# Performance work log

Measured on AMD Instinct MI355X. Metric: run time of the kernel, lower is better.

The kernel has to match this reference:

```python
import jax, jax.numpy as jnp
from jax import lax
import numpy as np

T, N, H, E, R, L, VOCAB = 512, 200, 64, 16, 10, 2, 200


def setup_inputs() -> dict:
    key = jax.random.key(0)
    ks = jax.random.split(key, 20)
    s = 0.1
    return {
        "inputs": jax.random.normal(ks[0], (T, N), jnp.float32),
        "indices": jnp.arange(N, dtype=jnp.int64) % VOCAB,
        "embed_W": jax.random.normal(ks[1], (VOCAB, E), jnp.float32),
        "Wih0": jax.random.normal(ks[2], (4 * H, 1), jnp.float32) * s,
        "Whh0": jax.random.normal(ks[3], (4 * H, H), jnp.float32) * s,
        "bih0": jax.random.normal(ks[4], (4 * H,), jnp.float32) * s,
        "bhh0": jax.random.normal(ks[5], (4 * H,), jnp.float32) * s,
        "Wih1": jax.random.normal(ks[6], (4 * H, H), jnp.float32) * s,
        "Whh1": jax.random.normal(ks[7], (4 * H, H), jnp.float32) * s,
        "bih1": jax.random.normal(ks[8], (4 * H,), jnp.float32) * s,
        "bhh1": jax.random.normal(ks[9], (4 * H,), jnp.float32) * s,
        "Wm": jax.random.normal(ks[10], (H + E, 1), jnp.float32) * s,
        "bm": jnp.zeros((1,), jnp.float32),
        "Wv": jax.random.normal(ks[11], (H + E, R), jnp.float32) * s,
        "bv": jnp.zeros((R,), jnp.float32),
        "Wd": jax.random.normal(ks[12], (H + E, 1), jnp.float32) * s,
        "bd": jnp.zeros((1,), jnp.float32),
    }


def _cell(x, h, c, Wih, Whh, bih, bhh):
    # PyTorch LSTM cell, gate order i, f, g, o
    g = x @ Wih.T + bih + h @ Whh.T + bhh
    i, f, gg, o = jnp.split(g, 4, axis=-1)
    c_new = jax.nn.sigmoid(f) * c + jax.nn.sigmoid(i) * jnp.tanh(gg)
    h_new = jax.nn.sigmoid(o) * jnp.tanh(c_new)
    return h_new, c_new


def reference(inputs, indices, embed_W, Wih0, Whh0, bih0, bhh0,
              Wih1, Whh1, bih1, bhh1, Wm, bm, Wv, bv, Wd, bd):
    Tn, Nn = inputs.shape
    Hh = Whh0.shape[1]
    layers = [(Wih0, Whh0, bih0, bhh0), (Wih1, Whh1, bih1, bhh1)]
    h0 = jnp.zeros((len(layers), Nn, Hh), inputs.dtype)
    c0 = jnp.zeros_like(h0)

    def step(carry, x_t):
        h, c = carry              # [L, N, H]
        x = x_t[:, None]          # [N, 1] -- assets batched along batch dim
        hs, cs = [], []
        for l, (Wih, Whh, bih, bhh) in enumerate(layers):
            hn, cn = _cell(x, h[l], c[l], Wih, Whh, bih, bhh)
            hs.append(hn)
            cs.append(cn)
            x = hn
        return (jnp.stack(hs), jnp.stack(cs)), x

    _, out = lax.scan(step, (h0, c0), inputs)          # [T, N, H]
    emb = embed_W[indices]                              # [N, E]
    y = jnp.concatenate(
        [out, jnp.broadcast_to(emb[None], (Tn,) + emb.shape)], axis=-1
    )                                                   # [T, N, H+E]
    mu_t = y @ Wm + bm                                  # [T, N, 1]
    d_t = jax.nn.softplus(y @ Wd + bd)[..., 0]          # [T, N]
    v_t = y @ Wv + bv                                   # [T, N, R]
    eye = jnp.eye(Nn, dtype=inputs.dtype)
    cov_t = jnp.einsum('tnr,tmr->tnm', v_t, v_t) + d_t[:, :, None] * eye
    return mu_t, cov_t
```

## Files before the change

### kernel.cpp

```cpp
#include <hip/hip_runtime.h>
#include <hip/hip_bf16.h>
#include <math.h>

#define TT 512
#define NN 200
#define HH 64
#define EE 16
#define RR 10
#define MU_OFF 0
#define COV_OFF (TT*NN)
#define HBLK (NN*NN)
#define HPAD 68

__device__ __forceinline__ float sigmoidf_(float x) {
    return 1.0f / (1.0f + __expf(-x));
}
__device__ __forceinline__ float tanhf_(float x) {
    x = fminf(15.0f, fmaxf(-15.0f, x));
    float e = __expf(2.0f * x);
    return (e - 1.0f) / (e + 1.0f);
}
__device__ __forceinline__ float act_(float g, bool is_tanh) {
    float xx = is_tanh ? 2.0f * g : g;
    float e = __expf(-xx);
    float v = 1.0f / (1.0f + e);
    return is_tanh ? fmaf(2.0f, v, -1.0f) : v;
}

__device__ __forceinline__ float dppxor1(float v) {
    return __int_as_float(__builtin_amdgcn_mov_dpp(__float_as_int(v), 0xB1, 0xf, 0xf, true));
}
__device__ __forceinline__ float dppxor2(float v) {
    return __int_as_float(__builtin_amdgcn_mov_dpp(__float_as_int(v), 0x4E, 0xf, 0xf, true));
}

#define BAR() do { asm volatile("s_waitcnt lgkmcnt(0)" ::: "memory"); \
                   __builtin_amdgcn_s_barrier();                      \
                   asm volatile("" ::: "memory"); } while (0)

#define PIN4(v) asm volatile("" : "+v"(v.x), "+v"(v.y), "+v"(v.z), "+v"(v.w))
#define RM4(M) M(0) M(1) M(2) M(3)

__global__
__attribute__((amdgpu_flat_work_group_size(512, 512), amdgpu_waves_per_eu(2, 2)))
void lstm_kernel(
    const float* __restrict__ inputs,
    const float* __restrict__ Wih0, const float* __restrict__ Whh0,
    const float* __restrict__ bih0, const float* __restrict__ bhh0,
    const float* __restrict__ Wih1, const float* __restrict__ Whh1,
    const float* __restrict__ bih1, const float* __restrict__ bhh1,
    float* __restrict__ out)
{
    const int n = blockIdx.x;
    const int tid = threadIdx.x;

    __shared__ float xs[TT];
    __shared__ float h0s[HH];
    __shared__ float h1s[HH];
    __shared__ float ga0[256];
    __shared__ float ga1[256];
    __shared__ float hist[64][HPAD];

    xs[tid] = inputs[tid * NN + n];
    if (tid < HH) { h0s[tid] = 0.0f; h1s[tid] = 0.0f; }

    float* covbase = out + COV_OFF + n * HH;

    if (tid < 256) {
        const int b4 = tid & ~3;
        const int qr = tid & 3;
#define DECLA(m) \
        float4 wA##m##_0, wA##m##_1, wA##m##_2, wA##m##_3; \
        { const float4* p = (const float4*)(Whh0 + (b4 + m) * HH + qr * 16); \
          wA##m##_0 = p[0]; wA##m##_1 = p[1]; wA##m##_2 = p[2]; wA##m##_3 = p[3]; \
          PIN4(wA##m##_0); PIN4(wA##m##_1); PIN4(wA##m##_2); PIN4(wA##m##_3); }
        RM4(DECLA)
#define DECLAB(m) const float wx##m = Wih0[b4 + m]; \
                  const float bb##m = bih0[b4 + m] + bhh0[b4 + m];
        RM4(DECLAB)
        const bool is_t = ((tid >> 6) == 2);
        const bool upd = (tid < HH);
        float c0 = 0.0f;

        BAR();

        for (int t = 0; t <= TT; ++t) {
            if (t < TT) {
                const float x = xs[t];
                const float4* hq = (const float4*)(h0s + qr * 16);
                float4 hc0 = hq[0], hc1 = hq[1], hc2 = hq[2], hc3 = hq[3];
                float acc0, acc1, acc2, acc3;
#define MVA(m) { \
                float a = (qr == 0) ? fmaf(wx##m, x, bb##m) : 0.0f; \
                a = fmaf(wA##m##_0.x, hc0.x, a); \
                a = fmaf(wA##m##_0.y, hc0.y, a); \
                a = fmaf(wA##m##_0.z, hc0.z, a); \
                a = fmaf(wA##m##_0.w, hc0.w, a); \
                a = fmaf(wA##m##_1.x, hc1.x, a); \
                a = fmaf(wA##m##_1.y, hc1.y, a); \
                a = fmaf(wA##m##_1.z, hc1.z, a); \
                a = fmaf(wA##m##_1.w, hc1.w, a); \
                a = fmaf(wA##m##_2.x, hc2.x, a); \
                a = fmaf(wA##m##_2.y, hc2.y, a); \
                a = fmaf(wA##m##_2.z, hc2.z, a); \
                a = fmaf(wA##m##_2.w, hc2.w, a); \
                a = fmaf(wA##m##_3.x, hc3.x, a); \
                a = fmaf(wA##m##_3.y, hc3.y, a); \
                a = fmaf(wA##m##_3.z, hc3.z, a); \
                a = fmaf(wA##m##_3.w, hc3.w, a); \
                acc##m = a; }
                RM4(MVA)
                acc0 += dppxor1(acc0); acc0 += dppxor2(acc0);
                acc1 += dppxor1(acc1); acc1 += dppxor2(acc1);
                acc2 += dppxor1(acc2); acc2 += dppxor2(acc2);
                acc3 += dppxor1(acc3); acc3 += dppxor2(acc3);
                float g = (qr == 0) ? acc0 : (qr == 1) ? acc1 : (qr == 2) ? acc2 : acc3;
                ga0[tid] = act_(g, is_t);
            }
            BAR();
            if (t < TT && upd) {
                float ia = ga0[tid], fa = ga0[tid + 64];
                float gg = ga0[tid + 128], oa = ga0[tid + 192];
                c0 = fmaf(fa, c0, ia * gg);
                h0s[tid] = oa * tanhf_(c0);
            }
            BAR();
            if ((t & 63) == 0 && t > 0) {
                const int s = tid >> 3;
                const int c = (tid & 7) * 8;
                float4 v0 = *(const float4*)&hist[s][c];
                float4 v1 = *(const float4*)&hist[s][c + 4];
                float* dst = covbase + (size_t)(t - 64 + s) * HBLK + c;
                ((float4*)dst)[0] = v0;
                ((float4*)dst)[1] = v1;
            }
        }
    } else {
        const int r = tid - 256;
        const int b4 = r & ~3;
        const int qr = r & 3;
#define DECLB(m) \
        float4 wI##m##_0, wI##m##_1, wI##m##_2, wI##m##_3; \
        float4 wH##m##_0, wH##m##_1, wH##m##_2, wH##m##_3; \
        { const float4* p = (const float4*)(Wih1 + (b4 + m) * HH + qr * 16); \
          wI##m##_0 = p[0]; wI##m##_1 = p[1]; wI##m##_2 = p[2]; wI##m##_3 = p[3]; \
          PIN4(wI##m##_0); PIN4(wI##m##_1); PIN4(wI##m##_2); PIN4(wI##m##_3); \
          const float4* q2 = (const float4*)(Whh1 + (b4 + m) * HH + qr * 16); \
          wH##m##_0 = q2[0]; wH##m##_1 = q2[1]; wH##m##_2 = q2[2]; wH##m##_3 = q2[3]; \
          PIN4(wH##m##_0); PIN4(wH##m##_1); PIN4(wH##m##_2); PIN4(wH##m##_3); }
        RM4(DECLB)
#define DECLBB(m) const float bB##m = bih1[b4 + m] + bhh1[b4 + m];
        RM4(DECLBB)
        const bool is_t = ((r >> 6) == 2);
        const bool upd = (r < HH);
        float c1 = 0.0f;

        BAR();

        for (int t = 0; t <= TT; ++t) {
            if (t >= 1) {
                const float4* hq = (const float4*)(h0s + qr * 16);
                const float4* gq = (const float4*)(h1s + qr * 16);
                float4 xc0 = hq[0], xc1 = hq[1], xc2 = hq[2], xc3 = hq[3];
                float4 yc0 = gq[0], yc1 = gq[1], yc2 = gq[2], yc3 = gq[3];
                float acc0, acc1, acc2, acc3;
#define MVB(m) { \
                float a = (qr == 0) ? bB##m : 0.0f; \
                float s2 = 0.0f; \
                a  = fmaf(wI##m##_0.x, xc0.x, a); \
                a  = fmaf(wI##m##_0.y, xc0.y, a); \
                a  = fmaf(wI##m##_0.z, xc0.z, a); \
                a  = fmaf(wI##m##_0.w, xc0.w, a); \
                a  = fmaf(wI##m##_1.x, xc1.x, a); \
                a  = fmaf(wI##m##_1.y, xc1.y, a); \
                a  = fmaf(wI##m##_1.z, xc1.z, a); \
                a  = fmaf(wI##m##_1.w, xc1.w, a); \
                a  = fmaf(wI##m##_2.x, xc2.x, a); \
                a  = fmaf(wI##m##_2.y, xc2.y, a); \
                a  = fmaf(wI##m##_2.z, xc2.z, a); \
                a  = fmaf(wI##m##_2.w, xc2.w, a); \
                a  = fmaf(wI##m##_3.x, xc3.x, a); \
                a  = fmaf(wI##m##_3.y, xc3.y, a); \
                a  = fmaf(wI##m##_3.z, xc3.z, a); \
                a  = fmaf(wI##m##_3.w, xc3.w, a); \
                s2 = fmaf(wH##m##_0.x, yc0.x, s2); \
                s2 = fmaf(wH##m##_0.y, yc0.y, s2); \
                s2 = fmaf(wH##m##_0.z, yc0.z, s2); \
                s2 = fmaf(wH##m##_0.w, yc0.w, s2); \
                s2 = fmaf(wH##m##_1.x, yc1.x, s2); \
                s2 = fmaf(wH##m##_1.y, yc1.y, s2); \
                s2 = fmaf(wH##m##_1.z, yc1.z, s2); \
                s2 = fmaf(wH##m##_1.w, yc1.w, s2); \
                s2 = fmaf(wH##m##_2.x, yc2.x, s2); \
                s2 = fmaf(wH##m##_2.y, yc2.y, s2); \
                s2 = fmaf(wH##m##_2.z, yc2.z, s2); \
                s2 = fmaf(wH##m##_2.w, yc2.w, s2); \
                s2 = fmaf(wH##m##_3.x, yc3.x, s2); \
                s2 = fmaf(wH##m##_3.y, yc3.y, s2); \
                s2 = fmaf(wH##m##_3.z, yc3.z, s2); \
                s2 = fmaf(wH##m##_3.w, yc3.w, s2); \
                acc##m = a + s2; }
                RM4(MVB)
                acc0 += dppxor1(acc0); acc0 += dppxor2(acc0);
                acc1 += dppxor1(acc1); acc1 += dppxor2(acc1);
                acc2 += dppxor1(acc2); acc2 += dppxor2(acc2);
                acc3 += dppxor1(acc3); acc3 += dppxor2(acc3);
                float g = (qr == 0) ? acc0 : (qr == 1) ? acc1 : (qr == 2) ? acc2 : acc3;
                ga1[r] = act_(g, is_t);
            }
            BAR();
            if (t >= 1 && upd) {
                float ia = ga1[r], fa = ga1[r + 64];
                float gg = ga1[r + 128], oa = ga1[r + 192];
                c1 = fmaf(fa, c1, ia * gg);
                float h1 = oa * tanhf_(c1);
                h1s[r] = h1;
                hist[(t - 1) & 63][r] = h1;
            }
            BAR();
            if ((t & 63) == 0 && t > 0) {
                const int s = tid >> 3;
                const int c = (tid & 7) * 8;
                float4 v0 = *(const float4*)&hist[s][c];
                float4 v1 = *(const float4*)&hist[s][c + 4];
                float* dst = covbase + (size_t)(t - 64 + s) * HBLK + c;
                ((float4*)dst)[0] = v0;
                ((float4*)dst)[1] = v1;
            }
        }
    }
}

__global__ __launch_bounds__(256) void head_kernel(
    const float* __restrict__ embW, const int* __restrict__ indices,
    const float* __restrict__ Wm, const float* __restrict__ bm,
    const float* __restrict__ Wv, const float* __restrict__ bv,
    const float* __restrict__ Wd, const float* __restrict__ bd,
    float* __restrict__ out)
{
    const int t = blockIdx.x;
    const int tid = threadIdx.x;

    __shared__ float hs[NN * HH];
    __shared__ float embs[NN * EE];
    __shared__ float Wvs[(HH + EE) * RR];
    __shared__ float Wms[HH + EE];
    __shared__ float Wds[HH + EE];
    __shared__ float Vs[NN * (RR + 1)];
    __shared__ float dsh[NN];
    __shared__ float bvs[RR];

    const float* hsrc = out + COV_OFF + (size_t)t * HBLK;
    for (int i = tid; i < (NN * HH) / 4; i += 256)
        ((float4*)hs)[i] = ((const float4*)hsrc)[i];
    for (int i = tid; i < NN * EE; i += 256) {
        int n = i >> 4, e = i & 15;
        embs[i] = embW[indices[n] * EE + e];
    }
    for (int i = tid; i < (HH + EE) * RR; i += 256) Wvs[i] = Wv[i];
    if (tid < HH + EE) { Wms[tid] = Wm[tid]; Wds[tid] = Wd[tid]; }
    if (tid < RR) bvs[tid] = bv[tid];
    __syncthreads();

    for (int p = tid; p < NN * RR; p += 256) {
        int n = p / RR, r = p - n * RR;
        const float* hn = hs + n * HH;
        const float* en = embs + n * EE;
        float acc = bvs[r];
#pragma unroll 8
        for (int k = 0; k < HH; ++k) acc = fmaf(hn[k], Wvs[k * RR + r], acc);
#pragma unroll
        for (int k = 0; k < EE; ++k) acc = fmaf(en[k], Wvs[(HH + k) * RR + r], acc);
        Vs[n * (RR + 1) + r] = acc;
    }
    const float bmv = bm[0], bdv = bd[0];
    for (int n = tid; n < NN; n += 256) {
        const float* hn = hs + n * HH;
        const float* en = embs + n * EE;
        float am = bmv, ad = bdv;
#pragma unroll 8
        for (int k = 0; k < HH; ++k) {
            float h = hn[k];
            am = fmaf(h, Wms[k], am);
            ad = fmaf(h, Wds[k], ad);
        }
#pragma unroll
        for (int k = 0; k < EE; ++k) {
            float e = en[k];
            am = fmaf(e, Wms[HH + k], am);
            ad = fmaf(e, Wds[HH + k], ad);
        }
        out[MU_OFF + t * NN + n] = am;
        dsh[n] = (ad > 20.0f) ? ad : log1pf(__expf(ad));
    }
    __syncthreads();

    float* covp = out + COV_OFF + (size_t)t * HBLK;
    for (int p = tid; p < NN * NN; p += 256) {
        int n = p / NN, m = p - n * NN;
        const float* vn = Vs + n * (RR + 1);
        const float* vm = Vs + m * (RR + 1);
        float acc = (n == m) ? dsh[n] : 0.0f;
#pragma unroll
        for (int r = 0; r < RR; ++r) acc = fmaf(vn[r], vm[r], acc);
        covp[p] = acc;
    }
}

extern "C" void kernel_launch(void* const* d_in, const int* in_sizes, int n_in,
                              void* d_out, int out_size, void* d_ws, size_t ws_size,
                              hipStream_t stream) {
    const float* inputs  = (const float*)d_in[0];
    const int*   indices = (const int*)d_in[1];
    const float* embW    = (const float*)d_in[2];
    const float* Wih0    = (const float*)d_in[3];
    const float* Whh0    = (const float*)d_in[4];
    const float* bih0    = (const float*)d_in[5];
    const float* bhh0    = (const float*)d_in[6];
    const float* Wih1    = (const float*)d_in[7];
    const float* Whh1    = (const float*)d_in[8];
    const float* bih1    = (const float*)d_in[9];
    const float* bhh1    = (const float*)d_in[10];
    const float* Wm      = (const float*)d_in[11];
    const float* bm      = (const float*)d_in[12];
    const float* Wv      = (const float*)d_in[13];
    const float* bv      = (const float*)d_in[14];
    const float* Wd      = (const float*)d_in[15];
    const float* bd      = (const float*)d_in[16];
    float* out = (float*)d_out;

    lstm_kernel<<<NN, 512, 0, stream>>>(inputs, Wih0, Whh0, bih0, bhh0,
                                        Wih1, Whh1, bih1, bhh1, out);
    head_kernel<<<TT, 256, 0, stream>>>(embW, indices, Wm, bm, Wv, bv, Wd, bd, out);
}
```

Measured before the change: 387.3 us.

## Remap LSTM gates per lane and double-buffer hidden state to halve barriers

Each group of four lanes now computes all four gates (i,f,g,o) for one hidden unit, so the cell update happens in registers right after the DPP reduction. This removes the shared gate buffers and the second barrier per timestep, and ping-pong buffers for h0/h1 avoid read/write races. The staged 64-step history buffer and its bulk float4 flush are replaced by direct scalar global stores of h1 each step. In exchange all four lanes of a group redundantly evaluate five transcendentals, and the output stores become small and uncoalesced.

```diff
diff --git a/kernel.cpp b/kernel.cpp
--- a/kernel.cpp
+++ b/kernel.cpp
@@ -10,7 +10,6 @@
 #define MU_OFF 0
 #define COV_OFF (TT*NN)
 #define HBLK (NN*NN)
-#define HPAD 68
 
 __device__ __forceinline__ float sigmoidf_(float x) {
     return 1.0f / (1.0f + __expf(-x));
@@ -19,12 +18,6 @@
     x = fminf(15.0f, fmaxf(-15.0f, x));
     float e = __expf(2.0f * x);
     return (e - 1.0f) / (e + 1.0f);
-}
-__device__ __forceinline__ float act_(float g, bool is_tanh) {
-    float xx = is_tanh ? 2.0f * g : g;
-    float e = __expf(-xx);
-    float v = 1.0f / (1.0f + e);
-    return is_tanh ? fmaf(2.0f, v, -1.0f) : v;
 }
 
 __device__ __forceinline__ float dppxor1(float v) {
@@ -51,43 +44,42 @@
     const float* __restrict__ bih1, const float* __restrict__ bhh1,
     float* __restrict__ out)
 {
-    const int n = blockIdx.x;
+    const int n   = blockIdx.x;
     const int tid = threadIdx.x;
 
     __shared__ float xs[TT];
-    __shared__ float h0s[HH];
-    __shared__ float h1s[HH];
-    __shared__ float ga0[256];
-    __shared__ float ga1[256];
-    __shared__ float hist[64][HPAD];
+    __shared__ float h0s[2][HH];
+    __shared__ float h1s[2][HH];
 
     xs[tid] = inputs[tid * NN + n];
-    if (tid < HH) { h0s[tid] = 0.0f; h1s[tid] = 0.0f; }
+    if (tid < HH) {
+        h0s[0][tid] = 0.0f; h0s[1][tid] = 0.0f;
+        h1s[0][tid] = 0.0f; h1s[1][tid] = 0.0f;
+    }
 
     float* covbase = out + COV_OFF + n * HH;
 
     if (tid < 256) {
-        const int b4 = tid & ~3;
+        const int j  = tid >> 2;
         const int qr = tid & 3;
 #define DECLA(m) \
         float4 wA##m##_0, wA##m##_1, wA##m##_2, wA##m##_3; \
-        { const float4* p = (const float4*)(Whh0 + (b4 + m) * HH + qr * 16); \
+        { const float4* p = (const float4*)(Whh0 + (j + 64*m) * HH + qr * 16); \
           wA##m##_0 = p[0]; wA##m##_1 = p[1]; wA##m##_2 = p[2]; wA##m##_3 = p[3]; \
           PIN4(wA##m##_0); PIN4(wA##m##_1); PIN4(wA##m##_2); PIN4(wA##m##_3); }
         RM4(DECLA)
-#define DECLAB(m) const float wx##m = Wih0[b4 + m]; \
-                  const float bb##m = bih0[b4 + m] + bhh0[b4 + m];
-        RM4(DECLAB)
-        const bool is_t = ((tid >> 6) == 2);
-        const bool upd = (tid < HH);
+#define DECLAC(m) const float wx##m = Wih0[j + 64*m]; \
+                  const float bb##m = bih0[j + 64*m] + bhh0[j + 64*m];
+        RM4(DECLAC)
         float c0 = 0.0f;
 
         BAR();
 
         for (int t = 0; t <= TT; ++t) {
             if (t < TT) {
+                const int rp = t & 1;
                 const float x = xs[t];
-                const float4* hq = (const float4*)(h0s + qr * 16);
+                const float4* hq = (const float4*)(&h0s[rp][qr * 16]);
                 float4 hc0 = hq[0], hc1 = hq[1], hc2 = hq[2], hc3 = hq[3];
                 float acc0, acc1, acc2, acc3;
 #define MVA(m) { \
@@ -114,55 +106,41 @@
                 acc1 += dppxor1(acc1); acc1 += dppxor2(acc1);
                 acc2 += dppxor1(acc2); acc2 += dppxor2(acc2);
                 acc3 += dppxor1(acc3); acc3 += dppxor2(acc3);
-                float g = (qr == 0) ? acc0 : (qr == 1) ? acc1 : (qr == 2) ? acc2 : acc3;
-                ga0[tid] = act_(g, is_t);
+                float ia = sigmoidf_(acc0), fa = sigmoidf_(acc1);
+                float ga = tanhf_(acc2),    oa = sigmoidf_(acc3);
+                c0 = fmaf(fa, c0, ia * ga);
+                float h0n = oa * tanhf_(c0);
+                if (qr == 0) h0s[rp ^ 1][j] = h0n;
             }
             BAR();
-            if (t < TT && upd) {
-                float ia = ga0[tid], fa = ga0[tid + 64];
-                float gg = ga0[tid + 128], oa = ga0[tid + 192];
-                c0 = fmaf(fa, c0, ia * gg);
-                h0s[tid] = oa * tanhf_(c0);
-            }
-            BAR();
-            if ((t & 63) == 0 && t > 0) {
-                const int s = tid >> 3;
-                const int c = (tid & 7) * 8;
-                float4 v0 = *(const float4*)&hist[s][c];
-                float4 v1 = *(const float4*)&hist[s][c + 4];
-                float* dst = covbase + (size_t)(t - 64 + s) * HBLK + c;
-                ((float4*)dst)[0] = v0;
-                ((float4*)dst)[1] = v1;
-            }
         }
     } else {
-        const int r = tid - 256;
-        const int b4 = r & ~3;
+        const int r  = tid - 256;
+        const int j  = r >> 2;
         const int qr = r & 3;
 #define DECLB(m) \
         float4 wI##m##_0, wI##m##_1, wI##m##_2, wI##m##_3; \
         float4 wH##m##_0, wH##m##_1, wH##m##_2, wH##m##_3; \
-        { const float4* p = (const float4*)(Wih1 + (b4 + m) * HH + qr * 16); \
+        { const float4* p = (const float4*)(Wih1 + (j + 64*m) * HH + qr * 16); \
           wI##m##_0 = p[0]; wI##m##_1 = p[1]; wI##m##_2 = p[2]; wI##m##_3 = p[3]; \
           PIN4(wI##m##_0); PIN4(wI##m##_1); PIN4(wI##m##_2); PIN4(wI##m##_3); \
-          const float4* q2 = (const float4*)(Whh1 + (b4 + m) * HH + qr * 16); \
+          const float4* q2 = (const float4*)(Whh1 + (j + 64*m) * HH + qr * 16); \
           wH##m##_0 = q2[0]; wH##m##_1 = q2[1]; wH##m##_2 = q2[2]; wH##m##_3 = q2[3]; \
           PIN4(wH##m##_0); PIN4(wH##m##_1); PIN4(wH##m##_2); PIN4(wH##m##_3); }
         RM4(DECLB)
-#define DECLBB(m) const float bB##m = bih1[b4 + m] + bhh1[b4 + m];
-        RM4(DECLBB)
-        const bool is_t = ((r >> 6) == 2);
-        const bool upd = (r < HH);
+#define DECLBC(m) const float bB##m = bih1[j + 64*m] + bhh1[j + 64*m];
+        RM4(DECLBC)
         float c1 = 0.0f;
 
         BAR();
 
         for (int t = 0; t <= TT; ++t) {
             if (t >= 1) {
-                const float4* hq = (const float4*)(h0s + qr * 16);
-                const float4* gq = (const float4*)(h1s + qr * 16);
-                float4 xc0 = hq[0], xc1 = hq[1], xc2 = hq[2], xc3 = hq[3];
-                float4 yc0 = gq[0], yc1 = gq[1], yc2 = gq[2], yc3 = gq[3];
+                const int rp = t & 1;
+                const float4* xq = (const float4*)(&h0s[rp][qr * 16]);
+                const float4* yq = (const float4*)(&h1s[rp][qr * 16]);
+                float4 xc0 = xq[0], xc1 = xq[1], xc2 = xq[2], xc3 = xq[3];
+                float4 yc0 = yq[0], yc1 = yq[1], yc2 = yq[2], yc3 = yq[3];
                 float acc0, acc1, acc2, acc3;
 #define MVB(m) { \
                 float a = (qr == 0) ? bB##m : 0.0f; \
@@ -205,28 +183,16 @@
                 acc1 += dppxor1(acc1); acc1 += dppxor2(acc1);
                 acc2 += dppxor1(acc2); acc2 += dppxor2(acc2);
                 acc3 += dppxor1(acc3); acc3 += dppxor2(acc3);
-                float g = (qr == 0) ? acc0 : (qr == 1) ? acc1 : (qr == 2) ? acc2 : acc3;
-                ga1[r] = act_(g, is_t);
+                float ia = sigmoidf_(acc0), fa = sigmoidf_(acc1);
+                float ga = tanhf_(acc2),    oa = sigmoidf_(acc3);
+                c1 = fmaf(fa, c1, ia * ga);
+                float h1n = oa * tanhf_(c1);
+                if (qr == 0) {
+                    h1s[rp ^ 1][j] = h1n;
+                    covbase[(size_t)(t - 1) * HBLK + j] = h1n;
+                }
             }
             BAR();
-            if (t >= 1 && upd) {
-                float ia = ga1[r], fa = ga1[r + 64];
-                float gg = ga1[r + 128], oa = ga1[r + 192];
-                c1 = fmaf(fa, c1, ia * gg);
-                float h1 = oa * tanhf_(c1);
-                h1s[r] = h1;
-                hist[(t - 1) & 63][r] = h1;
-            }
-            BAR();
-            if ((t & 63) == 0 && t > 0) {
-                const int s = tid >> 3;
-                const int c = (tid & 7) * 8;
-                float4 v0 = *(const float4*)&hist[s][c];
-                float4 v1 = *(const float4*)&hist[s][c + 4];
-                float* dst = covbase + (size_t)(t - 64 + s) * HBLK + c;
-                ((float4*)dst)[0] = v0;
-                ((float4*)dst)[1] = v1;
-            }
         }
     }
 }
```

Measured after the change: 466.6 us. 1.2x slower.

## Process two assets per LSTM block to amortize barriers and weight registers

Applied to the files above, without the earlier changes.

Each workgroup now runs the two-layer LSTM recurrence for two assets (n and n+100) at once, reusing the register-resident weights for both matvecs and sharing each step's barriers. The grid is halved to 100 blocks, and history flushing is split so layer-0 threads write asset A's history while layer-1 threads write asset B's. This amortizes the per-step synchronization latency that dominates the serial recurrence, at the cost of more ALU work per step and longer per-step critical paths on half as many CUs.

```diff
diff --git a/kernel.cpp b/kernel.cpp
--- a/kernel.cpp
+++ b/kernel.cpp
@@ -51,20 +51,26 @@
     const float* __restrict__ bih1, const float* __restrict__ bhh1,
     float* __restrict__ out)
 {
-    const int n = blockIdx.x;
+    const int na  = blockIdx.x;
+    const int nb  = blockIdx.x + 100;
     const int tid = threadIdx.x;
 
-    __shared__ float xs[TT];
-    __shared__ float h0s[HH];
-    __shared__ float h1s[HH];
-    __shared__ float ga0[256];
-    __shared__ float ga1[256];
-    __shared__ float hist[64][HPAD];
-
-    xs[tid] = inputs[tid * NN + n];
-    if (tid < HH) { h0s[tid] = 0.0f; h1s[tid] = 0.0f; }
-
-    float* covbase = out + COV_OFF + n * HH;
+    __shared__ float xsa[TT], xsb[TT];
+    __shared__ float h0sa[HH], h0sb[HH], h1sa[HH], h1sb[HH];
+    __shared__ float ga0a[256], ga0b[256];
+    __shared__ float ga1a[256], ga1b[256];
+    __shared__ float hista[64][HPAD];
+    __shared__ float histb[64][HPAD];
+
+    xsa[tid] = inputs[tid * NN + na];
+    xsb[tid] = inputs[tid * NN + nb];
+    if (tid < HH) {
+        h0sa[tid] = 0.0f; h0sb[tid] = 0.0f;
+        h1sa[tid] = 0.0f; h1sb[tid] = 0.0f;
+    }
+
+    float* covA = out + COV_OFF + na * HH;
+    float* covB = out + COV_OFF + nb * HH;
 
     if (tid < 256) {
         const int b4 = tid & ~3;
@@ -75,21 +81,16 @@
           wA##m##_0 = p[0]; wA##m##_1 = p[1]; wA##m##_2 = p[2]; wA##m##_3 = p[3]; \
           PIN4(wA##m##_0); PIN4(wA##m##_1); PIN4(wA##m##_2); PIN4(wA##m##_3); }
         RM4(DECLA)
-#define DECLAB(m) const float wx##m = Wih0[b4 + m]; \
+#define DECLAC(m) const float wx##m = Wih0[b4 + m]; \
                   const float bb##m = bih0[b4 + m] + bhh0[b4 + m];
-        RM4(DECLAB)
+        RM4(DECLAC)
         const bool is_t = ((tid >> 6) == 2);
-        const bool upd = (tid < HH);
         float c0 = 0.0f;
 
         BAR();
 
         for (int t = 0; t <= TT; ++t) {
             if (t < TT) {
-                const float x = xs[t];
-                const float4* hq = (const float4*)(h0s + qr * 16);
-                float4 hc0 = hq[0], hc1 = hq[1], hc2 = hq[2], hc3 = hq[3];
-                float acc0, acc1, acc2, acc3;
 #define MVA(m) { \
                 float a = (qr == 0) ? fmaf(wx##m, x, bb##m) : 0.0f; \
                 a = fmaf(wA##m##_0.x, hc0.x, a); \
@@ -109,34 +110,63 @@
                 a = fmaf(wA##m##_3.z, hc3.z, a); \
                 a = fmaf(wA##m##_3.w, hc3.w, a); \
                 acc##m = a; }
-                RM4(MVA)
-                acc0 += dppxor1(acc0); acc0 += dppxor2(acc0);
-                acc1 += dppxor1(acc1); acc1 += dppxor2(acc1);
-                acc2 += dppxor1(acc2); acc2 += dppxor2(acc2);
-                acc3 += dppxor1(acc3); acc3 += dppxor2(acc3);
-                float g = (qr == 0) ? acc0 : (qr == 1) ? acc1 : (qr == 2) ? acc2 : acc3;
-                ga0[tid] = act_(g, is_t);
+                {
+                    const float x = xsa[t];
+                    const float4* hq = (const float4*)(h0sa + qr * 16);
+                    float4 hc0 = hq[0], hc1 = hq[1], hc2 = hq[2], hc3 = hq[3];
+                    float acc0, acc1, acc2, acc3;
+                    RM4(MVA)
+                    acc0 += dppxor1(acc0); acc0 += dppxor2(acc0);
+                    acc1 += dppxor1(acc1); acc1 += dppxor2(acc1);
+                    acc2 += dppxor1(acc2); acc2 += dppxor2(acc2);
+                    acc3 += dppxor1(acc3); acc3 += dppxor2(acc3);
+                    float g = (qr == 0) ? acc0 : (qr == 1) ? acc1 : (qr == 2) ? acc2 : acc3;
+                    ga0a[tid] = act_(g, is_t);
+                }
+                {
+                    const float x = xsb[t];
+                    const float4* hq = (const float4*)(h0sb + qr * 16);
+                    float4 hc0 = hq[0], hc1 = hq[1], hc2 = hq[2], hc3 = hq[3];
+                    float acc0, acc1, acc2, acc3;
+                    RM4(MVA)
+                    acc0 += dppxor1(acc0); acc0 += dppxor2(acc0);
+                    acc1 += dppxor1(acc1); acc1 += dppxor2(acc1);
+                    acc2 += dppxor1(acc2); acc2 += dppxor2(acc2);
+                    acc3 += dppxor1(acc3); acc3 += dppxor2(acc3);
+                    float g = (qr == 0) ? acc0 : (qr == 1) ? acc1 : (qr == 2) ? acc2 : acc3;
+                    ga0b[tid] = act_(g, is_t);
+                }
             }
             BAR();
-            if (t < TT && upd) {
-                float ia = ga0[tid], fa = ga0[tid + 64];
-                float gg = ga0[tid + 128], oa = ga0[tid + 192];
-                c0 = fmaf(fa, c0, ia * gg);
-                h0s[tid] = oa * tanhf_(c0);
+            if (t < TT) {
+                if (tid < 64) {
+                    float ia = ga0a[tid], fa = ga0a[tid + 64];
+                    float gg = ga0a[tid + 128], oa = ga0a[tid + 192];
+                    c0 = fmaf(fa, c0, ia * gg);
+                    h0sa[tid] = oa * tanhf_(c0);
+                } else if (tid < 128) {
+                    const int j = tid - 64;
+                    float ia = ga0b[j], fa = ga0b[j + 64];
+                    float gg = ga0b[j + 128], oa = ga0b[j + 192];
+                    c0 = fmaf(fa, c0, ia * gg);
+                    h0sb[j] = oa * tanhf_(c0);
+                }
             }
             BAR();
             if ((t & 63) == 0 && t > 0) {
-                const int s = tid >> 3;
-                const int c = (tid & 7) * 8;
-                float4 v0 = *(const float4*)&hist[s][c];
-                float4 v1 = *(const float4*)&hist[s][c + 4];
-                float* dst = covbase + (size_t)(t - 64 + s) * HBLK + c;
-                ((float4*)dst)[0] = v0;
-                ((float4*)dst)[1] = v1;
+                const int s = tid >> 2;
+                const int c = (tid & 3) * 16;
+                float4 v0 = *(const float4*)&hista[s][c];
+                float4 v1 = *(const float4*)&hista[s][c + 4];
+                float4 v2 = *(const float4*)&hista[s][c + 8];
+                float4 v3 = *(const float4*)&hista[s][c + 12];
+                float* dst = covA + (size_t)(t - 64 + s) * HBLK + c;
+                ((float4*)dst)[0] = v0; ((float4*)dst)[1] = v1;
+                ((float4*)dst)[2] = v2; ((float4*)dst)[3] = v3;
             }
         }
     } else {
-        const int r = tid - 256;
+        const int r  = tid - 256;
         const int b4 = r & ~3;
         const int qr = r & 3;
 #define DECLB(m) \
@@ -149,21 +179,15 @@
           wH##m##_0 = q2[0]; wH##m##_1 = q2[1]; wH##m##_2 = q2[2]; wH##m##_3 = q2[3]; \
           PIN4(wH##m##_0); PIN4(wH##m##_1); PIN4(wH##m##_2); PIN4(wH##m##_3); }
         RM4(DECLB)
-#define DECLBB(m) const float bB##m = bih1[b4 + m] + bhh1[b4 + m];
-        RM4(DECLBB)
+#define DECLBC(m) const float bB##m = bih1[b4 + m] + bhh1[b4 + m];
+        RM4(DECLBC)
         const bool is_t = ((r >> 6) == 2);
-        const bool upd = (r < HH);
         float c1 = 0.0f;
 
         BAR();
 
         for (int t = 0; t <= TT; ++t) {
             if (t >= 1) {
-                const float4* hq = (const float4*)(h0s + qr * 16);
-                const float4* gq = (const float4*)(h1s + qr * 16);
-                float4 xc0 = hq[0], xc1 = hq[1], xc2 = hq[2], xc3 = hq[3];
-                float4 yc0 = gq[0], yc1 = gq[1], yc2 = gq[2], yc3 = gq[3];
-                float acc0, acc1, acc2, acc3;
 #define MVB(m) { \
                 float a = (qr == 0) ? bB##m : 0.0f; \
                 float s2 = 0.0f; \
@@ -200,32 +224,65 @@
                 s2 = fmaf(wH##m##_3.z, yc3.z, s2); \
                 s2 = fmaf(wH##m##_3.w, yc3.w, s2); \
                 acc##m = a + s2; }
-                RM4(MVB)
-                acc0 += dppxor1(acc0); acc0 += dppxor2(acc0);
-                acc1 += dppxor1(acc1); acc1 += dppxor2(acc1);
-                acc2 += dppxor1(acc2); acc2 += dppxor2(acc2);
-                acc3 += dppxor1(acc3); acc3 += dppxor2(acc3);
-                float g = (qr == 0) ? acc0 : (qr == 1) ? acc1 : (qr == 2) ? acc2 : acc3;
-                ga1[r] = act_(g, is_t);
+                {
+                    const float4* xq = (const float4*)(h0sa + qr * 16);
+                    const float4* yq = (const float4*)(h1sa + qr * 16);
+                    float4 xc0 = xq[0], xc1 = xq[1], xc2 = xq[2], xc3 = xq[3];
+                    float4 yc0 = yq[0], yc1 = yq[1], yc2 = yq[2], yc3 = yq[3];
+                    float acc0, acc1, acc2, acc3;
+                    RM4(MVB)
+                    acc0 += dppxor1(acc0); acc0 += dppxor2(acc0);
+                    acc1 += dppxor1(acc1); acc1 += dppxor2(acc1);
+                    acc2 += dppxor1(acc2); acc2 += dppxor2(acc2);
+                    acc3 += dppxor1(acc3); acc3 += dppxor2(acc3);
+                    float g = (qr == 0) ? acc0 : (qr == 1) ? acc1 : (qr == 2) ? acc2 : acc3;
+                    ga1a[r] = act_(g, is_t);
+                }
+                {
+                    const float4* xq = (const float4*)(h0sb + qr * 16);
+                    const float4* yq = (const float4*)(h1sb + qr * 16);
+                    float4 xc0 = xq[0], xc1 = xq[1], xc2 = xq[2], xc3 = xq[3];
+                    float4 yc0 = yq[0], yc1 = yq[1], yc2 = yq[2], yc3 = yq[3];
+                    float acc0, acc1, acc2, acc3;
+                    RM4(MVB)
+                    acc0 += dppxor1(acc0); acc0 += dppxor2(acc0);
+                    acc1 += dppxor1(acc1); acc1 += dppxor2(acc1);
+                    acc2 += dppxor1(acc2); acc2 += dppxor2(acc2);
+                    acc3 += dppxor1(acc3); acc3 += dppxor2(acc3);
+                    float g = (qr == 0) ? acc0 : (qr == 1) ? acc1 : (qr == 2) ? acc2 : acc3;
+                    ga1b[r] = act_(g, is_t);
+                }
             }
             BAR();
-            if (t >= 1 && upd) {
-                float ia = ga1[r], fa = ga1[r + 64];
-                float gg = ga1[r + 128], oa = ga1[r + 192];
-                c1 = fmaf(fa, c1, ia * gg);
-                float h1 = oa * tanhf_(c1);
-                h1s[r] = h1;
-                hist[(t - 1) & 63][r] = h1;
+            if (t >= 1) {
+                if (r < 64) {
+                    float ia = ga1a[r], fa = ga1a[r + 64];
+                    float gg = ga1a[r + 128], oa = ga1a[r + 192];
+                    c1 = fmaf(fa, c1, ia * gg);
+                    float h1 = oa * tanhf_(c1);
+                    h1sa[r] = h1;
+                    hista[(t - 1) & 63][r] = h1;
+                } else if (r < 128) {
+                    const int j = r - 64;
+                    float ia = ga1b[j], fa = ga1b[j + 64];
+                    float gg = ga1b[j + 128], oa = ga1b[j + 192];
+                    c1 = fmaf(fa, c1, ia * gg);
+                    float h1 = oa * tanhf_(c1);
+                    h1sb[j] = h1;
+                    histb[(t - 1) & 63][j] = h1;
+                }
             }
             BAR();
             if ((t & 63) == 0 && t > 0) {
-                const int s = tid >> 3;
-                const int c = (tid & 7) * 8;
-                float4 v0 = *(const float4*)&hist[s][c];
-                float4 v1 = *(const float4*)&hist[s][c + 4];
-                float* dst = covbase + (size_t)(t - 64 + s) * HBLK + c;
-                ((float4*)dst)[0] = v0;
-                ((float4*)dst)[1] = v1;
+                const int s = r >> 2;
+                const int c = (r & 3) * 16;
+                float4 v0 = *(const float4*)&histb[s][c];
+                float4 v1 = *(const float4*)&histb[s][c + 4];
+                float4 v2 = *(const float4*)&histb[s][c + 8];
+                float4 v3 = *(const float4*)&histb[s][c + 12];
+                float* dst = covB + (size_t)(t - 64 + s) * HBLK + c;
+                ((float4*)dst)[0] = v0; ((float4*)dst)[1] = v1;
+                ((float4*)dst)[2] = v2; ((float4*)dst)[3] = v3;
             }
         }
     }
@@ -329,7 +386,7 @@
     const float* bd      = (const float*)d_in[16];
     float* out = (float*)d_out;
 
-    lstm_kernel<<<NN, 512, 0, stream>>>(inputs, Wih0, Whh0, bih0, bhh0,
-                                        Wih1, Whh1, bih1, bhh1, out);
+    lstm_kernel<<<NN / 2, 512, 0, stream>>>(inputs, Wih0, Whh0, bih0, bhh0,
+                                            Wih1, Whh1, bih1, bhh1, out);
     head_kernel<<<TT, 256, 0, stream>>>(embW, indices, Wm, bm, Wv, bv, Wd, bd, out);
 }
```

Result: slower. 679.5 us (+75.4%).
